# Kernel optimization log

Measured on AMD Instinct MI355X. Metric: run time of the kernel, lower is better.

The kernel has to match this reference:

```python
import jax, jax.numpy as jnp
import numpy as np


def setup_inputs() -> dict:
    key = jax.random.key(0)
    k1, k2 = jax.random.split(key)
    b, c, h, w = 16, 512, 64, 64
    rgb_feat = jax.random.normal(k1, (b, c, h, w), dtype=jnp.float32)
    depth_feat = jax.random.normal(k2, (b, c, h, w), dtype=jnp.float32)
    return {"rgb_feat": rgb_feat, "depth_feat": depth_feat}


def reference(rgb_feat, depth_feat):
    b, c, h, w = rgb_feat.shape
    rgb_r = rgb_feat.reshape(b, c, h * w)      # (b, c, hw)
    depth_r = depth_feat.reshape(b, c, h * w)  # (b, c, hw)
    # interaction: (b, c, c) = depth_r @ rgb_r^T
    interaction = jnp.einsum('bcs,bds->bcd', depth_r, rgb_r)
    interaction = jax.nn.sigmoid(interaction)
    # depth_weighted: (b, c, hw) = interaction @ depth_r
    depth_weighted = jnp.einsum('bcd,bds->bcs', interaction, depth_r)
    fused = rgb_feat + depth_weighted.reshape(b, c, h, w)
    return fused
```

## Files before the change

### kernel.cpp

```cpp
#include <hip/hip_runtime.h>

#define B_ 16
#define C_ 512
#define S_ 4096

typedef __attribute__((ext_vector_type(4))) float float4v;
typedef __attribute__((ext_vector_type(8))) short short8;
typedef __attribute__((ext_vector_type(4))) short short4v;

typedef __attribute__((address_space(1))) unsigned int as1_uint;
typedef __attribute__((address_space(3))) unsigned int as3_uint;

#define ASYNC16(gsrc, ldst) \
  __builtin_amdgcn_global_load_lds((as1_uint*)(gsrc), (as3_uint*)(ldst), 16, 0, 0)

#define PIPE_SYNC(N)                                              \
  do {                                                            \
    asm volatile("s_waitcnt vmcnt(" #N ")\n\ts_barrier" ::: "memory"); \
    __builtin_amdgcn_sched_barrier(0);                            \
  } while (0)

__device__ __forceinline__ unsigned short f2bf(float f) {
  unsigned u = __builtin_bit_cast(unsigned, f);
  u = u + 0x7FFFu + ((u >> 16) & 1u);
  return (unsigned short)(u >> 16);
}

__global__ __launch_bounds__(256) void k_prep(
    const float* __restrict__ depth, const float* __restrict__ rgb,
    unsigned short* __restrict__ depthN, unsigned short* __restrict__ rgbN,
    unsigned short* __restrict__ depthT) {
  __shared__ __align__(16) unsigned short tT[64][72];
  int b = blockIdx.z;
  int s0 = blockIdx.x * 64, d0 = blockIdx.y * 64;
  int t = threadIdx.x;
  size_t base = ((size_t)(b * C_ + d0)) * S_ + s0;
#pragma unroll
  for (int it = 0; it < 4; ++it) {
    int slot = it * 256 + t;
    int d = slot >> 4, l16 = slot & 15;
    size_t off = (size_t)d * S_ + l16 * 4;
    float4v v = *(const float4v*)(depth + base + off);
    unsigned short e0 = f2bf(v.x), e1 = f2bf(v.y), e2 = f2bf(v.z),
                   e3 = f2bf(v.w);
    short4v o = {(short)e0, (short)e1, (short)e2, (short)e3};
    *(short4v*)(depthN + base + off) = o;
    int ss = l16 * 4;
    tT[ss + 0][(((d >> 3) ^ ((ss + 0) & 7)) << 3) + (d & 7)] = e0;
    tT[ss + 1][(((d >> 3) ^ ((ss + 1) & 7)) << 3) + (d & 7)] = e1;
    tT[ss + 2][(((d >> 3) ^ ((ss + 2) & 7)) << 3) + (d & 7)] = e2;
    tT[ss + 3][(((d >> 3) ^ ((ss + 3) & 7)) << 3) + (d & 7)] = e3;
    float4v u = *(const float4v*)(rgb + base + off);
    short4v o2 = {(short)f2bf(u.x), (short)f2bf(u.y), (short)f2bf(u.z),
                  (short)f2bf(u.w)};
    *(short4v*)(rgbN + base + off) = o2;
  }
  __syncthreads();
  unsigned short* dT = depthT + ((size_t)(b * S_ + s0)) * C_ + d0;
#pragma unroll
  for (int it = 0; it < 2; ++it) {
    int slot = it * 256 + t;
    int s = slot >> 3, g = slot & 7;
    short8 vv = *(const short8*)&tT[s][(g ^ (s & 7)) << 3];
    *(short8*)(dT + (size_t)s * C_ + g * 8) = vv;
  }
}

__global__ __launch_bounds__(256) void k_gemm1(
    const unsigned short* __restrict__ depthN,
    const unsigned short* __restrict__ rgbN, unsigned short* __restrict__ I) {
  __shared__ __align__(16) short As[3][64 * 64];
  __shared__ __align__(16) short Bs[3][128 * 64];
  int lid = blockIdx.x + 8 * (blockIdx.y + 4 * blockIdx.z);
  int swz = (lid & 7) * 64 + (lid >> 3);
  int bx = swz & 7, by = (swz >> 3) & 3, b = swz >> 5;
  int c0 = bx * 64, d0 = by * 128;
  int t = threadIdx.x;
  const unsigned short* An = depthN + ((size_t)(b * C_ + c0)) * S_;
  const unsigned short* Bn = rgbN + ((size_t)(b * C_ + d0)) * S_;
  int w = t >> 6, l = t & 63, half = l >> 4, r = l & 15;
  int wm = (w >> 1) * 32, wn = (w & 1) * 64;
  float4v acc[2][4] = {};

  auto stage = [&](int bi, int k0) {
#pragma unroll
    for (int q = 0; q < 2; ++q) {
      int idx = q * 256 + t, row = idx >> 3, ch = (idx & 7) ^ (row & 7);
      ASYNC16(An + (size_t)row * S_ + k0 + ch * 8, &As[bi][idx * 8]);
    }
#pragma unroll
    for (int q = 0; q < 4; ++q) {
      int idx = q * 256 + t, row = idx >> 3, ch = (idx & 7) ^ (row & 7);
      ASYNC16(Bn + (size_t)row * S_ + k0 + ch * 8, &Bs[bi][idx * 8]);
    }
  };

  stage(0, 0);
  stage(1, 64);
  stage(2, 128);
  PIPE_SYNC(12);

  const int NKT = S_ / 64;
  for (int kt = 0; kt < NKT; ++kt) {
    int cur = kt % 3;
    short8 af[2][2], bfr[4][2];
#pragma unroll
    for (int i = 0; i < 2; ++i) {
      int row = wm + 16 * i + r;
#pragma unroll
      for (int kk = 0; kk < 2; ++kk)
        af[i][kk] = *(const short8*)&As[cur][row * 64 +
                                            (((kk * 4 + half) ^ (row & 7)) * 8)];
    }
#pragma unroll
    for (int j = 0; j < 4; ++j) {
      int row = wn + 16 * j + r;
#pragma unroll
      for (int kk = 0; kk < 2; ++kk)
        bfr[j][kk] = *(const short8*)&Bs[cur][row * 64 +
                                             (((kk * 4 + half) ^ (row & 7)) * 8)];
    }
    __builtin_amdgcn_s_setprio(1);
#pragma unroll
    for (int kk = 0; kk < 2; ++kk)
#pragma unroll
      for (int i = 0; i < 2; ++i)
#pragma unroll
        for (int j = 0; j < 4; ++j)
          acc[i][j] = __builtin_amdgcn_mfma_f32_16x16x32_bf16(
              af[i][kk], bfr[j][kk], acc[i][j], 0, 0, 0);
    __builtin_amdgcn_s_setprio(0);
    if (kt + 2 < NKT) {
      PIPE_SYNC(6);
    } else if (kt + 1 < NKT) {
      PIPE_SYNC(0);
    }
    if (kt + 3 < NKT) stage(cur, (kt + 3) * 64);
  }

#pragma unroll
  for (int i = 0; i < 2; ++i)
#pragma unroll
    for (int j = 0; j < 4; ++j)
#pragma unroll
      for (int reg = 0; reg < 4; ++reg) {
        int c = c0 + wm + 16 * i + half * 4 + reg;
        int d = d0 + wn + 16 * j + r;
        float g = 1.0f / (1.0f + __expf(-acc[i][j][reg]));
        I[((size_t)(b * C_ + c)) * C_ + d] = f2bf(g);
      }
}

__global__ __launch_bounds__(256) void k_gemm2(
    const unsigned short* __restrict__ I,
    const unsigned short* __restrict__ depthT, const float* __restrict__ rgb,
    float* __restrict__ out) {
  __shared__ __align__(16) short As[3][128 * 32];
  __shared__ __align__(16) short Bs[3][128 * 32];
  int lid = blockIdx.x + 4 * (blockIdx.y + 32 * blockIdx.z);
  int swz = (lid & 7) * 256 + (lid >> 3);
  int bx = swz & 3, by = (swz >> 2) & 31, b = swz >> 7;
  int c0 = bx * 128, s0 = by * 128;
  int t = threadIdx.x;
  const unsigned short* Ab = I + ((size_t)(b * C_ + c0)) * C_;
  const unsigned short* Bb = depthT + ((size_t)(b * S_ + s0)) * C_;
  int w = t >> 6, l = t & 63, half = l >> 4, r = l & 15;
  int wm = (w >> 1) * 64, wn = (w & 1) * 64;
  float4v acc[4][4] = {};

  auto stage = [&](int bi, int k0) {
#pragma unroll
    for (int q = 0; q < 2; ++q) {
      int idx = q * 256 + t, row = idx >> 2, ch = (idx & 3) ^ (row & 3);
      ASYNC16(Ab + (size_t)row * C_ + k0 + ch * 8, &As[bi][idx * 8]);
      ASYNC16(Bb + (size_t)row * C_ + k0 + ch * 8, &Bs[bi][idx * 8]);
    }
  };

  stage(0, 0);
  stage(1, 32);
  stage(2, 64);
  PIPE_SYNC(8);

  const int NKT = C_ / 32;
  for (int kt = 0; kt < NKT; ++kt) {
    int cur = kt % 3;
    short8 af[4], bfr[4];
#pragma unroll
    for (int i = 0; i < 4; ++i) {
      int rowa = wm + 16 * i + r;
      af[i] = *(const short8*)&As[cur][rowa * 32 +
                                       (((half ^ (rowa & 3)) & 3) * 8)];
      int rowb = wn + 16 * i + r;
      bfr[i] = *(const short8*)&Bs[cur][rowb * 32 +
                                        (((half ^ (rowb & 3)) & 3) * 8)];
    }
    __builtin_amdgcn_s_setprio(1);
#pragma unroll
    for (int i = 0; i < 4; ++i)
#pragma unroll
      for (int j = 0; j < 4; ++j)
        acc[i][j] = __builtin_amdgcn_mfma_f32_16x16x32_bf16(af[i], bfr[j],
                                                            acc[i][j], 0, 0, 0);
    __builtin_amdgcn_s_setprio(0);
    if (kt + 2 < NKT) {
      PIPE_SYNC(4);
    } else if (kt + 1 < NKT) {
      PIPE_SYNC(0);
    }
    if (kt + 3 < NKT) stage(cur, (kt + 3) * 32);
  }

#pragma unroll
  for (int i = 0; i < 4; ++i)
#pragma unroll
    for (int j = 0; j < 4; ++j)
#pragma unroll
      for (int reg = 0; reg < 4; ++reg) {
        int c = c0 + wm + 16 * i + half * 4 + reg;
        int s = s0 + wn + 16 * j + r;
        size_t o = ((size_t)(b * C_ + c)) * S_ + s;
        out[o] = rgb[o] + acc[i][j][reg];
      }
}

extern "C" void kernel_launch(void* const* d_in, const int* in_sizes, int n_in,
                              void* d_out, int out_size, void* d_ws,
                              size_t ws_size, hipStream_t stream) {
  const float* rgb = (const float*)d_in[0];
  const float* depth = (const float*)d_in[1];
  float* out = (float*)d_out;
  unsigned short* depthT = (unsigned short*)d_ws;
  unsigned short* I =
      (unsigned short*)((char*)d_ws + (size_t)B_ * S_ * C_ * 2);
  unsigned short* depthN = (unsigned short*)d_out;
  unsigned short* rgbN = depthN + (size_t)B_ * C_ * S_;

  k_prep<<<dim3(S_ / 64, C_ / 64, B_), 256, 0, stream>>>(depth, rgb, depthN,
                                                         rgbN, depthT);
  k_gemm1<<<dim3(C_ / 64, C_ / 128, B_), 256, 0, stream>>>(depthN, rgbN, I);
  k_gemm2<<<dim3(C_ / 128, S_ / 128, B_), 256, 0, stream>>>(I, depthT, rgb,
                                                            out);
}
```

Measured before the change: 499.4 us.

## Split prep into convert and transpose kernels and enlarge GEMM tiles

The fused prep kernel is split in two. One is a flat, vectorised fp32-to-bf16 conversion of both inputs. The other is a separate transpose that rereads depthN from global memory and uses an unswizzled, padded LDS tile. GEMM1 goes from a 64x128 to a 128x128 block tile, and GEMM2 goes from 128x128 to a 256x64 tile, each with matching changes to staging and waitcnt. The goal is more operand reuse per block and a simpler prep, at the cost of an extra launch, an extra read of depthN, and more LDS and registers per GEMM block.

```diff
diff --git a/kernel.cpp b/kernel.cpp
--- a/kernel.cpp
+++ b/kernel.cpp
@@ -14,10 +14,10 @@
 #define ASYNC16(gsrc, ldst) \
   __builtin_amdgcn_global_load_lds((as1_uint*)(gsrc), (as3_uint*)(ldst), 16, 0, 0)
 
-#define PIPE_SYNC(N)                                              \
-  do {                                                            \
+#define PIPE_SYNC(N)                                                   \
+  do {                                                                 \
     asm volatile("s_waitcnt vmcnt(" #N ")\n\ts_barrier" ::: "memory"); \
-    __builtin_amdgcn_sched_barrier(0);                            \
+    __builtin_amdgcn_sched_barrier(0);                                 \
   } while (0)
 
 __device__ __forceinline__ unsigned short f2bf(float f) {
@@ -26,65 +26,76 @@
   return (unsigned short)(u >> 16);
 }
 
-__global__ __launch_bounds__(256) void k_prep(
+__global__ __launch_bounds__(256) void k_conv(
     const float* __restrict__ depth, const float* __restrict__ rgb,
-    unsigned short* __restrict__ depthN, unsigned short* __restrict__ rgbN,
+    unsigned short* __restrict__ depthN, unsigned short* __restrict__ rgbN) {
+  int half = blockIdx.x >> 11;
+  const float* src = half ? rgb : depth;
+  unsigned short* dst = half ? rgbN : depthN;
+  size_t tid = ((size_t)(blockIdx.x & 2047)) * 256 + threadIdx.x;
+#pragma unroll
+  for (int it = 0; it < 8; ++it) {
+    size_t c = tid + (size_t)it * 524288;
+    const float* p = src + c * 8;
+    float4v v0 = *(const float4v*)p;
+    float4v v1 = *(const float4v*)(p + 4);
+    short8 o = {(short)f2bf(v0.x), (short)f2bf(v0.y), (short)f2bf(v0.z),
+                (short)f2bf(v0.w), (short)f2bf(v1.x), (short)f2bf(v1.y),
+                (short)f2bf(v1.z), (short)f2bf(v1.w)};
+    *(short8*)(dst + c * 8) = o;
+  }
+}
+
+__global__ __launch_bounds__(256) void k_trans(
+    const unsigned short* __restrict__ depthN,
     unsigned short* __restrict__ depthT) {
-  __shared__ __align__(16) unsigned short tT[64][72];
+  __shared__ __align__(16) unsigned short tT[64][68];
   int b = blockIdx.z;
   int s0 = blockIdx.x * 64, d0 = blockIdx.y * 64;
   int t = threadIdx.x;
-  size_t base = ((size_t)(b * C_ + d0)) * S_ + s0;
-#pragma unroll
-  for (int it = 0; it < 4; ++it) {
+  const unsigned short* src = depthN + ((size_t)(b * C_ + d0)) * S_ + s0;
+#pragma unroll
+  for (int it = 0; it < 2; ++it) {
     int slot = it * 256 + t;
-    int d = slot >> 4, l16 = slot & 15;
-    size_t off = (size_t)d * S_ + l16 * 4;
-    float4v v = *(const float4v*)(depth + base + off);
-    unsigned short e0 = f2bf(v.x), e1 = f2bf(v.y), e2 = f2bf(v.z),
-                   e3 = f2bf(v.w);
-    short4v o = {(short)e0, (short)e1, (short)e2, (short)e3};
-    *(short4v*)(depthN + base + off) = o;
-    int ss = l16 * 4;
-    tT[ss + 0][(((d >> 3) ^ ((ss + 0) & 7)) << 3) + (d & 7)] = e0;
-    tT[ss + 1][(((d >> 3) ^ ((ss + 1) & 7)) << 3) + (d & 7)] = e1;
-    tT[ss + 2][(((d >> 3) ^ ((ss + 2) & 7)) << 3) + (d & 7)] = e2;
-    tT[ss + 3][(((d >> 3) ^ ((ss + 3) & 7)) << 3) + (d & 7)] = e3;
-    float4v u = *(const float4v*)(rgb + base + off);
-    short4v o2 = {(short)f2bf(u.x), (short)f2bf(u.y), (short)f2bf(u.z),
-                  (short)f2bf(u.w)};
-    *(short4v*)(rgbN + base + off) = o2;
+    int d = slot >> 3, c = slot & 7;
+    short8 v = *(const short8*)(src + (size_t)d * S_ + c * 8);
+    short4v lo = {v[0], v[1], v[2], v[3]};
+    short4v hi = {v[4], v[5], v[6], v[7]};
+    *(short4v*)&tT[d][c * 8] = lo;
+    *(short4v*)&tT[d][c * 8 + 4] = hi;
   }
   __syncthreads();
-  unsigned short* dT = depthT + ((size_t)(b * S_ + s0)) * C_ + d0;
+  unsigned short* dst = depthT + ((size_t)(b * S_ + s0)) * C_ + d0;
 #pragma unroll
   for (int it = 0; it < 2; ++it) {
     int slot = it * 256 + t;
     int s = slot >> 3, g = slot & 7;
-    short8 vv = *(const short8*)&tT[s][(g ^ (s & 7)) << 3];
-    *(short8*)(dT + (size_t)s * C_ + g * 8) = vv;
+    short8 o;
+#pragma unroll
+    for (int e = 0; e < 8; ++e) o[e] = (short)tT[g * 8 + e][s];
+    *(short8*)(dst + (size_t)s * C_ + g * 8) = o;
   }
 }
 
 __global__ __launch_bounds__(256) void k_gemm1(
     const unsigned short* __restrict__ depthN,
     const unsigned short* __restrict__ rgbN, unsigned short* __restrict__ I) {
-  __shared__ __align__(16) short As[3][64 * 64];
+  __shared__ __align__(16) short As[3][128 * 64];
   __shared__ __align__(16) short Bs[3][128 * 64];
-  int lid = blockIdx.x + 8 * (blockIdx.y + 4 * blockIdx.z);
-  int swz = (lid & 7) * 64 + (lid >> 3);
-  int bx = swz & 7, by = (swz >> 3) & 3, b = swz >> 5;
-  int c0 = bx * 64, d0 = by * 128;
+  int lid = blockIdx.x + 4 * blockIdx.y + 16 * blockIdx.z;
+  int swz = (lid & 7) * 32 + (lid >> 3);
+  int bx = swz & 3, by = (swz >> 2) & 3, b = swz >> 4;
+  int c0 = bx * 128, d0 = by * 128;
   int t = threadIdx.x;
   const unsigned short* An = depthN + ((size_t)(b * C_ + c0)) * S_;
   const unsigned short* Bn = rgbN + ((size_t)(b * C_ + d0)) * S_;
   int w = t >> 6, l = t & 63, half = l >> 4, r = l & 15;
-  int wm = (w >> 1) * 32, wn = (w & 1) * 64;
-  float4v acc[2][4] = {};
+  int wm = (w >> 1) * 64, wn = (w & 1) * 64;
+  float4v acc[4][4] = {};
 
   auto stage = [&](int bi, int k0) {
 #pragma unroll
-    for (int q = 0; q < 2; ++q) {
+    for (int q = 0; q < 4; ++q) {
       int idx = q * 256 + t, row = idx >> 3, ch = (idx & 7) ^ (row & 7);
       ASYNC16(An + (size_t)row * S_ + k0 + ch * 8, &As[bi][idx * 8]);
     }
@@ -98,14 +109,14 @@
   stage(0, 0);
   stage(1, 64);
   stage(2, 128);
-  PIPE_SYNC(12);
+  PIPE_SYNC(16);
 
   const int NKT = S_ / 64;
   for (int kt = 0; kt < NKT; ++kt) {
     int cur = kt % 3;
-    short8 af[2][2], bfr[4][2];
-#pragma unroll
-    for (int i = 0; i < 2; ++i) {
+    short8 af[4][2], bfr[4][2];
+#pragma unroll
+    for (int i = 0; i < 4; ++i) {
       int row = wm + 16 * i + r;
 #pragma unroll
       for (int kk = 0; kk < 2; ++kk)
@@ -124,14 +135,14 @@
 #pragma unroll
     for (int kk = 0; kk < 2; ++kk)
 #pragma unroll
-      for (int i = 0; i < 2; ++i)
+      for (int i = 0; i < 4; ++i)
 #pragma unroll
         for (int j = 0; j < 4; ++j)
           acc[i][j] = __builtin_amdgcn_mfma_f32_16x16x32_bf16(
               af[i][kk], bfr[j][kk], acc[i][j], 0, 0, 0);
     __builtin_amdgcn_s_setprio(0);
     if (kt + 2 < NKT) {
-      PIPE_SYNC(6);
+      PIPE_SYNC(8);
     } else if (kt + 1 < NKT) {
       PIPE_SYNC(0);
     }
@@ -139,7 +150,7 @@
   }
 
 #pragma unroll
-  for (int i = 0; i < 2; ++i)
+  for (int i = 0; i < 4; ++i)
 #pragma unroll
     for (int j = 0; j < 4; ++j)
 #pragma unroll
@@ -155,24 +166,27 @@
     const unsigned short* __restrict__ I,
     const unsigned short* __restrict__ depthT, const float* __restrict__ rgb,
     float* __restrict__ out) {
-  __shared__ __align__(16) short As[3][128 * 32];
-  __shared__ __align__(16) short Bs[3][128 * 32];
-  int lid = blockIdx.x + 4 * (blockIdx.y + 32 * blockIdx.z);
+  __shared__ __align__(16) short As[3][256 * 32];
+  __shared__ __align__(16) short Bs[3][64 * 32];
+  int lid = blockIdx.x + 2 * blockIdx.y + 128 * blockIdx.z;
   int swz = (lid & 7) * 256 + (lid >> 3);
-  int bx = swz & 3, by = (swz >> 2) & 31, b = swz >> 7;
-  int c0 = bx * 128, s0 = by * 128;
+  int bx = swz & 1, by = (swz >> 1) & 63, b = swz >> 7;
+  int c0 = bx * 256, s0 = by * 64;
   int t = threadIdx.x;
   const unsigned short* Ab = I + ((size_t)(b * C_ + c0)) * C_;
   const unsigned short* Bb = depthT + ((size_t)(b * S_ + s0)) * C_;
   int w = t >> 6, l = t & 63, half = l >> 4, r = l & 15;
-  int wm = (w >> 1) * 64, wn = (w & 1) * 64;
+  int wm = w * 64, wn = 0;
   float4v acc[4][4] = {};
 
   auto stage = [&](int bi, int k0) {
 #pragma unroll
-    for (int q = 0; q < 2; ++q) {
+    for (int q = 0; q < 4; ++q) {
       int idx = q * 256 + t, row = idx >> 2, ch = (idx & 3) ^ (row & 3);
       ASYNC16(Ab + (size_t)row * C_ + k0 + ch * 8, &As[bi][idx * 8]);
+    }
+    {
+      int idx = t, row = idx >> 2, ch = (idx & 3) ^ (row & 3);
       ASYNC16(Bb + (size_t)row * C_ + k0 + ch * 8, &Bs[bi][idx * 8]);
     }
   };
@@ -180,7 +194,7 @@
   stage(0, 0);
   stage(1, 32);
   stage(2, 64);
-  PIPE_SYNC(8);
+  PIPE_SYNC(10);
 
   const int NKT = C_ / 32;
   for (int kt = 0; kt < NKT; ++kt) {
@@ -189,11 +203,11 @@
 #pragma unroll
     for (int i = 0; i < 4; ++i) {
       int rowa = wm + 16 * i + r;
-      af[i] = *(const short8*)&As[cur][rowa * 32 +
-                                       (((half ^ (rowa & 3)) & 3) * 8)];
+      af[i] =
+          *(const short8*)&As[cur][rowa * 32 + (((half ^ (rowa & 3)) & 3) * 8)];
       int rowb = wn + 16 * i + r;
-      bfr[i] = *(const short8*)&Bs[cur][rowb * 32 +
-                                        (((half ^ (rowb & 3)) & 3) * 8)];
+      bfr[i] =
+          *(const short8*)&Bs[cur][rowb * 32 + (((half ^ (rowb & 3)) & 3) * 8)];
     }
     __builtin_amdgcn_s_setprio(1);
 #pragma unroll
@@ -204,7 +218,7 @@
                                                             acc[i][j], 0, 0, 0);
     __builtin_amdgcn_s_setprio(0);
     if (kt + 2 < NKT) {
-      PIPE_SYNC(4);
+      PIPE_SYNC(5);
     } else if (kt + 1 < NKT) {
       PIPE_SYNC(0);
     }
@@ -231,14 +245,12 @@
   const float* depth = (const float*)d_in[1];
   float* out = (float*)d_out;
   unsigned short* depthT = (unsigned short*)d_ws;
-  unsigned short* I =
-      (unsigned short*)((char*)d_ws + (size_t)B_ * S_ * C_ * 2);
+  unsigned short* I = (unsigned short*)((char*)d_ws + (size_t)B_ * S_ * C_ * 2);
   unsigned short* depthN = (unsigned short*)d_out;
   unsigned short* rgbN = depthN + (size_t)B_ * C_ * S_;
 
-  k_prep<<<dim3(S_ / 64, C_ / 64, B_), 256, 0, stream>>>(depth, rgb, depthN,
-                                                         rgbN, depthT);
-  k_gemm1<<<dim3(C_ / 64, C_ / 128, B_), 256, 0, stream>>>(depthN, rgbN, I);
-  k_gemm2<<<dim3(C_ / 128, S_ / 128, B_), 256, 0, stream>>>(I, depthT, rgb,
-                                                            out);
-}
+  k_conv<<<dim3(4096), 256, 0, stream>>>(depth, rgb, depthN, rgbN);
+  k_trans<<<dim3(S_ / 64, C_ / 64, B_), 256, 0, stream>>>(depthN, depthT);
+  k_gemm1<<<dim3(C_ / 128, C_ / 128, B_), 256, 0, stream>>>(depthN, rgbN, I);
+  k_gemm2<<<dim3(C_ / 256, S_ / 64, B_), 256, 0, stream>>>(I, depthT, rgb, out);
+}
```

New measurement: 537.1 us. +7.5%, slower.
